# Kernel optimization log

Measured on AMD Instinct MI355X. Metric: run time of the kernel, lower is better.

Reference implementation:

```python
import jax, jax.numpy as jnp
import numpy as np

B = 32768      # batch of head nodes
E = 1048576    # total edges (avg degree ~32)
DIM = 64
N_H, N_R, N_T = 3846, 60, 9366


def setup_inputs() -> dict:
    key = jax.random.key(0)
    k = jax.random.split(key, 7)
    h = jax.random.randint(k[0], (B,), 0, N_H)
    edge_seg = jnp.sort(jax.random.randint(k[1], (E,), 0, B))
    edge_rel = jax.random.randint(k[2], (E,), 0, N_R)
    edge_tail = jax.random.randint(k[3], (E,), 0, N_T)
    H_emb = jax.random.normal(k[4], (N_H, DIM), dtype=jnp.float32)
    R_emb = jax.random.normal(k[5], (N_R, DIM), dtype=jnp.float32)
    T_emb = jax.random.normal(k[6], (N_T, DIM), dtype=jnp.float32)
    return {"h": h, "edge_seg": edge_seg, "edge_rel": edge_rel,
            "edge_tail": edge_tail, "H_emb": H_emb, "R_emb": R_emb,
            "T_emb": T_emb}


def reference(h, edge_seg, edge_rel, edge_tail, H_emb, R_emb, T_emb):
    # Per-head embedding, gathered out to each of its edges.  [E, DIM]
    Hs = H_emb[h][edge_seg]
    R_v = R_emb[edge_rel]                  # [E, DIM]
    # Attention logits: dot(H_v[j], R_v[k]) per edge.  [E]
    scores = jnp.sum(Hs * R_v, axis=-1)
    # Segment (per-head) softmax over the ragged neighbor lists.
    m = jax.ops.segment_max(scores, edge_seg, num_segments=B)
    m = jnp.where(jnp.isfinite(m), m, jnp.float32(0.0))  # guard empty segs
    e = jnp.exp(scores - m[edge_seg])
    denom = jax.ops.segment_sum(e, edge_seg, num_segments=B)
    w = e / jnp.where(denom > 0, denom, jnp.float32(1.0))[edge_seg]
    # Original: Hv = (T_v - R_v) * score; V_New = sum over ALL elements
    # (a scalar), written into the whole row v_c[j].  Equivalently:
    contrib = w * jnp.sum(T_emb[edge_tail] - R_v, axis=-1)   # [E]
    vc_scalar = jax.ops.segment_sum(contrib, edge_seg, num_segments=B)  # [B]
    return jnp.broadcast_to(vc_scalar[:, None], (B, DIM))
```

## Files before the change

kernel.cpp:

```cpp
#include <hip/hip_runtime.h>
#include <hip/hip_fp16.h>
#include <math.h>


__global__ __launch_bounds__(256) void setup_k(
    const int* __restrict__ seg, int E, int B, int* __restrict__ seg_start,
    const float* __restrict__ H, const float* __restrict__ R,
    const float* __restrict__ T,
    float* __restrict__ P, __half* __restrict__ tsum, float* __restrict__ rsumg,
    int NH, int NR, int NT, int eBlocks, int sBlocks)
{
    int b   = blockIdx.x;
    int tid = threadIdx.x;

    if (b < eBlocks) {
        int e = b * 256 + tid;
        if (e < E) {
            int lane = tid & 63;
            int cur  = seg[e];
            int prev = __shfl_up(cur, 1, 64);
            if (lane == 0) prev = (e == 0) ? -1 : seg[e - 1];
            for (int s = prev + 1; s <= cur; ++s) seg_start[s] = e;
            if (e == E - 1)
                for (int s = cur + 1; s <= B; ++s) seg_start[s] = E;
        }
        return;
    }
    b -= eBlocks;

    if (b < sBlocks) {
        __shared__ float Rt[64 * 64];
        for (int t = tid; t < NR * 64; t += 256) {
            int r = t >> 6, d = t & 63;
            Rt[d * NR + r] = R[t];
        }
        __syncthreads();
        if (tid < NR) {
            float s = 0.f;
            #pragma unroll 8
            for (int d = 0; d < 64; ++d) s += Rt[d * NR + tid];
            if (b == 0) rsumg[tid] = s;
        }

        int idx = b * 256 + tid;
        if (idx < NH * NR) {
            int i = idx / NR;
            int r = idx - i * NR;
            const float4* h4 = (const float4*)(H + (size_t)i * 64);
            float acc = 0.f;
            #pragma unroll
            for (int q = 0; q < 16; ++q) {
                float4 hv = h4[q];
                int d = q * 4;
                acc = fmaf(hv.x, Rt[(d + 0) * NR + r], acc);
                acc = fmaf(hv.y, Rt[(d + 1) * NR + r], acc);
                acc = fmaf(hv.z, Rt[(d + 2) * NR + r], acc);
                acc = fmaf(hv.w, Rt[(d + 3) * NR + r], acc);
            }
            P[idx] = __expf(acc);
        }
        return;
    }
    b -= sBlocks;

    {
        int lane = tid & 63;
        int row  = b * 16 + (tid >> 6) * 4 + (lane >> 4);
        if (row < NT) {
            float4 v = ((const float4*)T)[(size_t)row * 16 + (lane & 15)];
            float s = v.x + v.y + v.z + v.w;
            s += __shfl_xor(s, 8, 64);
            s += __shfl_xor(s, 4, 64);
            s += __shfl_xor(s, 2, 64);
            s += __shfl_xor(s, 1, 64);
            if ((lane & 15) == 0) tsum[row] = __float2half(s);
        }
    }
}

#define TS_LDS_HALVES 9472
__global__ __launch_bounds__(256) void main_k(
    const int* __restrict__ h,
    const int* __restrict__ edge_rel, const int* __restrict__ edge_tail,
    const float* __restrict__ P, const __half* __restrict__ tsum,
    const float* __restrict__ rsumg, const int* __restrict__ seg_start,
    float* __restrict__ out, int B, int NR, int NT)
{
    __shared__ __half ts[TS_LDS_HALVES];
    __shared__ float  rs[64];
    int tid = threadIdx.x;

    {
        const uint4* src = (const uint4*)tsum;
        uint4*       dst = (uint4*)ts;
        int n16 = (NT * 2 + 15) >> 4;
        for (int i = tid; i < n16; i += 256) dst[i] = src[i];
    }
    if (tid < NR) rs[tid] = rsumg[tid];
    __syncthreads();

    int sub  = tid & 31;
    int grp0 = blockIdx.x * 32 + (tid >> 5);
    #pragma unroll
    for (int k = 0; k < 4; ++k) {
        int grp = grp0 + k * 8;
        if (grp >= B) break;
        int lo = seg_start[grp];
        int hi = seg_start[grp + 1];
        const float* Prow = P + (size_t)h[grp] * NR;

        float se = 0.f, sec = 0.f;
        for (int e = lo + sub; e < hi; e += 32) {
            int rel = edge_rel[e];
            int tl  = edge_tail[e];
            float pv = Prow[rel];
            float c  = __half2float(ts[tl]) - rs[rel];
            sec = fmaf(pv, c, sec);
            se += pv;
        }
        #pragma unroll
        for (int off = 16; off; off >>= 1) {
            se  += __shfl_xor(se, off, 64);
            sec += __shfl_xor(sec, off, 64);
        }
        float vc = (se > 0.f) ? (sec / se) : 0.f;
        *(float2*)(out + (size_t)grp * 64 + sub * 2) = make_float2(vc, vc);
    }
}

extern "C" void kernel_launch(void* const* d_in, const int* in_sizes, int n_in,
                              void* d_out, int out_size, void* d_ws, size_t ws_size,
                              hipStream_t stream)
{
    const int*   h     = (const int*)d_in[0];
    const int*   eseg  = (const int*)d_in[1];
    const int*   erel  = (const int*)d_in[2];
    const int*   etail = (const int*)d_in[3];
    const float* Hv    = (const float*)d_in[4];
    const float* Rv    = (const float*)d_in[5];
    const float* Tv    = (const float*)d_in[6];

    int B  = in_sizes[0];
    int E  = in_sizes[1];
    int NH = in_sizes[4] / 64;
    int NR = in_sizes[5] / 64;
    int NT = in_sizes[6] / 64;

    char*  ws  = (char*)d_ws;
    size_t off = 0;
    auto alloc = [&](size_t bytes) -> void* {
        void* q = ws + off;
        off = (off + bytes + 255) & ~(size_t)255;
        return q;
    };
    float*  P         = (float*) alloc((size_t)NH * NR * sizeof(float));
    __half* tsum      = (__half*)alloc((size_t)(NT + 128) * sizeof(__half));
    float*  rsumg     = (float*) alloc(64 * sizeof(float));
    int*    seg_start = (int*)   alloc((size_t)(B + 1) * sizeof(int));
    (void)ws_size;

    int eBlocks = (E + 255) / 256;
    int sBlocks = (NH * NR + 255) / 256;
    int tBlocks = (NT + 15) / 16;
    setup_k<<<eBlocks + sBlocks + tBlocks, 256, 0, stream>>>(
        eseg, E, B, seg_start, Hv, Rv, Tv, P, tsum, rsumg, NH, NR, NT,
        eBlocks, sBlocks);

    main_k<<<(B + 31) / 32, 256, 0, stream>>>(
        h, erel, etail, P, tsum, rsumg, seg_start, (float*)d_out, B, NR, NT);
}
```

Measured before the change: 24.79 us.

## Replace segment-start scan with per-block binary search; read fp32 tail sums from global

Segment boundaries are no longer built by a separate pass over all E edge segment ids in the setup kernel. Each main block now binary-searches the sorted edge_seg array for its 33 boundaries. The tail-sum table becomes fp32 and is read directly from global/L2 instead of being staged as fp16 into LDS by every block. This removes about 4MB of segment reads and the per-block LDS fill, at the cost of serial binary-search latency at block start and random global gathers for tail sums.

```diff
diff --git a/kernel.cpp b/kernel.cpp
--- a/kernel.cpp
+++ b/kernel.cpp
@@ -1,32 +1,15 @@
 #include <hip/hip_runtime.h>
-#include <hip/hip_fp16.h>
 #include <math.h>
 
 
 __global__ __launch_bounds__(256) void setup_k(
-    const int* __restrict__ seg, int E, int B, int* __restrict__ seg_start,
     const float* __restrict__ H, const float* __restrict__ R,
     const float* __restrict__ T,
-    float* __restrict__ P, __half* __restrict__ tsum, float* __restrict__ rsumg,
-    int NH, int NR, int NT, int eBlocks, int sBlocks)
+    float* __restrict__ P, float* __restrict__ tsum, float* __restrict__ rsumg,
+    int NH, int NR, int NT, int sBlocks)
 {
     int b   = blockIdx.x;
     int tid = threadIdx.x;
-
-    if (b < eBlocks) {
-        int e = b * 256 + tid;
-        if (e < E) {
-            int lane = tid & 63;
-            int cur  = seg[e];
-            int prev = __shfl_up(cur, 1, 64);
-            if (lane == 0) prev = (e == 0) ? -1 : seg[e - 1];
-            for (int s = prev + 1; s <= cur; ++s) seg_start[s] = e;
-            if (e == E - 1)
-                for (int s = cur + 1; s <= B; ++s) seg_start[s] = E;
-        }
-        return;
-    }
-    b -= eBlocks;
 
     if (b < sBlocks) {
         __shared__ float Rt[64 * 64];
@@ -35,11 +18,11 @@
             Rt[d * NR + r] = R[t];
         }
         __syncthreads();
-        if (tid < NR) {
+        if (b == 0 && tid < NR) {
             float s = 0.f;
             #pragma unroll 8
             for (int d = 0; d < 64; ++d) s += Rt[d * NR + tid];
-            if (b == 0) rsumg[tid] = s;
+            rsumg[tid] = s;
         }
 
         int idx = b * 256 + tid;
@@ -73,40 +56,44 @@
             s += __shfl_xor(s, 4, 64);
             s += __shfl_xor(s, 2, 64);
             s += __shfl_xor(s, 1, 64);
-            if ((lane & 15) == 0) tsum[row] = __float2half(s);
+            if ((lane & 15) == 0) tsum[row] = s;
         }
     }
 }
 
-#define TS_LDS_HALVES 9472
 __global__ __launch_bounds__(256) void main_k(
-    const int* __restrict__ h,
+    const int* __restrict__ h, const int* __restrict__ eseg,
     const int* __restrict__ edge_rel, const int* __restrict__ edge_tail,
-    const float* __restrict__ P, const __half* __restrict__ tsum,
-    const float* __restrict__ rsumg, const int* __restrict__ seg_start,
-    float* __restrict__ out, int B, int NR, int NT)
+    const float* __restrict__ P, const float* __restrict__ tsum,
+    const float* __restrict__ rsumg,
+    float* __restrict__ out, int B, int E, int NR)
 {
-    __shared__ __half ts[TS_LDS_HALVES];
-    __shared__ float  rs[64];
-    int tid = threadIdx.x;
+    __shared__ int   bounds[33];
+    __shared__ float rs[64];
+    int tid  = threadIdx.x;
+    int base = blockIdx.x * 32;
 
-    {
-        const uint4* src = (const uint4*)tsum;
-        uint4*       dst = (uint4*)ts;
-        int n16 = (NT * 2 + 15) >> 4;
-        for (int i = tid; i < n16; i += 256) dst[i] = src[i];
+    if (tid < NR) rs[tid] = rsumg[tid];
+    if (tid < 33) {
+        int s = base + tid;
+        int lo = 0, hi = E;
+        while (lo < hi) {
+            int mid = (lo + hi) >> 1;
+            if (eseg[mid] < s) lo = mid + 1; else hi = mid;
+        }
+        bounds[tid] = lo;
     }
-    if (tid < NR) rs[tid] = rsumg[tid];
     __syncthreads();
 
     int sub  = tid & 31;
-    int grp0 = blockIdx.x * 32 + (tid >> 5);
+    int gidx = tid >> 5;
     #pragma unroll
     for (int k = 0; k < 4; ++k) {
-        int grp = grp0 + k * 8;
+        int j   = gidx + k * 8;
+        int grp = base + j;
         if (grp >= B) break;
-        int lo = seg_start[grp];
-        int hi = seg_start[grp + 1];
+        int lo = bounds[j];
+        int hi = bounds[j + 1];
         const float* Prow = P + (size_t)h[grp] * NR;
 
         float se = 0.f, sec = 0.f;
@@ -114,7 +101,7 @@
             int rel = edge_rel[e];
             int tl  = edge_tail[e];
             float pv = Prow[rel];
-            float c  = __half2float(ts[tl]) - rs[rel];
+            float c  = tsum[tl] - rs[rel];
             sec = fmaf(pv, c, sec);
             se += pv;
         }
@@ -153,19 +140,16 @@
         off = (off + bytes + 255) & ~(size_t)255;
         return q;
     };
-    float*  P         = (float*) alloc((size_t)NH * NR * sizeof(float));
-    __half* tsum      = (__half*)alloc((size_t)(NT + 128) * sizeof(__half));
-    float*  rsumg     = (float*) alloc(64 * sizeof(float));
-    int*    seg_start = (int*)   alloc((size_t)(B + 1) * sizeof(int));
+    float* P     = (float*)alloc((size_t)NH * NR * sizeof(float));
+    float* tsum  = (float*)alloc((size_t)NT * sizeof(float));
+    float* rsumg = (float*)alloc(64 * sizeof(float));
     (void)ws_size;
 
-    int eBlocks = (E + 255) / 256;
     int sBlocks = (NH * NR + 255) / 256;
     int tBlocks = (NT + 15) / 16;
-    setup_k<<<eBlocks + sBlocks + tBlocks, 256, 0, stream>>>(
-        eseg, E, B, seg_start, Hv, Rv, Tv, P, tsum, rsumg, NH, NR, NT,
-        eBlocks, sBlocks);
+    setup_k<<<sBlocks + tBlocks, 256, 0, stream>>>(
+        Hv, Rv, Tv, P, tsum, rsumg, NH, NR, NT, sBlocks);
 
     main_k<<<(B + 31) / 32, 256, 0, stream>>>(
-        h, erel, etail, P, tsum, rsumg, seg_start, (float*)d_out, B, NR, NT);
+        h, eseg, erel, etail, P, tsum, rsumg, (float*)d_out, B, E, NR);
 }
```

Measured after the change: 23.30 us. 6.0% less time.
